# Performance work log

Hardware: AMD Instinct MI355X
Metric: run time of the kernel (lower is better)

Reference implementation:

```python
import jax, jax.numpy as jnp
import numpy as np

# Static problem sizes (uniform T/taus make the ragged edge list static).
B, N, F, T, TAU, S = 8, 384, 64, 192, 192, 5
SINK_SHIFT = T                    # min sink index == T (sinks are the new nodes)
N_SINK, N_SOURCE = TAU, T + TAU - 1


def _edge_indices():
    # tril_indices(T+tau, offset=-1), keep sink >= T  (window=None)
    r, c = np.tril_indices(T + TAU, k=-1)
    m = r >= T
    r, c = r[m], c[m]
    e = r.shape[0]
    batch = np.repeat(np.arange(B), e)
    return (jnp.asarray(batch, jnp.int32),
            jnp.asarray(np.tile(r, B), jnp.int32),
            jnp.asarray(np.tile(c, B), jnp.int32))


def setup_inputs() -> dict:
    key = jax.random.key(0)
    ks = jax.random.split(key, 6)
    batch_idx, sink_idx, source_idx = _edge_indices()
    s1, s2 = 1.0 / np.sqrt(2 * F), 1.0 / np.sqrt(F)
    return {
        "nodes": jax.random.normal(ks[0], (B, N, F), jnp.float32),
        "w1": jax.random.uniform(ks[1], (2 * F, F), jnp.float32, -s1, s1),
        "b1": jnp.zeros((F,), jnp.float32),
        "g1": jnp.ones((F,), jnp.float32),
        "be1": jnp.zeros((F,), jnp.float32),
        "w2": jax.random.uniform(ks[2], (F, F), jnp.float32, -s2, s2),
        "b2": jnp.zeros((F,), jnp.float32),
        "g2": jnp.ones((F,), jnp.float32),
        "be2": jnp.zeros((F,), jnp.float32),
        "w3": jax.random.uniform(ks[3], (F, 1), jnp.float32, -s2, s2),
        "b3": jnp.zeros((1,), jnp.float32),
        "gumbel": jax.random.gumbel(ks[4], (S, B, N_SINK, N_SOURCE), jnp.float32),
        "batch_idx": batch_idx,
        "sink_idx": sink_idx,
        "source_idx": source_idx,
    }


def _ln(x, g, b):
    mu = x.mean(-1, keepdims=True)
    v = ((x - mu) ** 2).mean(-1, keepdims=True)
    return (x - mu) * jax.lax.rsqrt(v + 1e-5) * g + b


def reference(nodes, w1, b1, g1, be1, w2, b2, g2, be2, w3, b3,
              gumbel, batch_idx, sink_idx, source_idx):
    # gather sink/source node pairs: [E, 2F]
    sink = nodes[batch_idx, sink_idx]
    src = nodes[batch_idx, source_idx]
    x = jnp.concatenate([sink, src], axis=-1)
    # edge MLP -> per-edge logit
    h = _ln(jax.nn.relu(x @ w1 + b1), g1, be1)
    h = _ln(jax.nn.relu(h @ w2 + b2), g2, be2)
    logits = (h @ w3 + b3)[:, 0]                     # [E]
    # dense-padded grid filled with finfo.min (as in torch)
    neg = jnp.finfo(jnp.float32).min
    gs = jnp.full((B, N_SINK, N_SOURCE), neg, jnp.float32)
    gs = gs.at[batch_idx, sink_idx - SINK_SHIFT, source_idx].set(logits)
    # hard gumbel-softmax over source dim, S independent samples
    y_soft = jax.nn.softmax(gs[None] + gumbel, axis=-1)      # [S,B,192,383]
    y_hard = jax.nn.one_hot(jnp.argmax(y_soft, -1), N_SOURCE, dtype=y_soft.dtype)
    y = y_soft + jax.lax.stop_gradient(y_hard - y_soft)
    e = y.sum(0)
    # straight-through binarize: forward (e>0), backward identity
    e = e + jax.lax.stop_gradient((e > 0).astype(e.dtype) - e)
    valid = e[batch_idx, sink_idx - SINK_SHIFT, source_idx]
    vals = jnp.where(valid > 0, valid, 0.0)
    # dense equivalent of the sparse COO adjacency (B, N, N)
    return jnp.zeros((B, N, N), jnp.float32).at[batch_idx, sink_idx, source_idx].set(vals)
```

## Files before the change

### kernel.cpp

```cpp
#include <hip/hip_runtime.h>
#include <math.h>
#include <stdint.h>

#define BB 8
#define NN 384
#define FF 64
#define TT 192
#define NSRC 383
#define NSINK 192
#define SS 5
#define NEDGE 441600
#define BN (BB * NN)
#define TILE_E 128
#define NBLKE (NEDGE / TILE_E)
#define OUTV ((BB * NN * NN) / 4)

typedef float f32x2 __attribute__((ext_vector_type(2)));

#if defined(__has_builtin) && __has_builtin(__builtin_elementwise_fma)
#define PKFMA(a, b, c) __builtin_elementwise_fma((a), (b), (c))
#else
#define PKFMA(a, b, c) ((a) * (b) + (c))
#endif

__global__ __launch_bounds__(64) void prep_all(
    const float* __restrict__ nodes, const float* __restrict__ w1,
    const float* __restrict__ b1,
    const float* __restrict__ w2, const float* __restrict__ b2,
    const float* __restrict__ g1, const float* __restrict__ be1,
    const float* __restrict__ g2, const float* __restrict__ be2,
    const float* __restrict__ w3, const float* __restrict__ b3,
    float* __restrict__ A, float* __restrict__ Bv,
    float* __restrict__ W2kj, float* __restrict__ wcol,
    float* __restrict__ cb, float* __restrict__ gw,
    float* __restrict__ cwsgw) {
  const int blk = blockIdx.x;
  const int k = threadIdx.x;
  if (blk < BN / 4) {
    const int bn0 = blk * 4;
    __shared__ float nd[4][FF];
#pragma unroll
    for (int i = 0; i < 4; ++i) nd[i][k] = nodes[(bn0 + i) * FF + k];
    __syncthreads();
    const float bk = b1[k];
    float a0 = bk, a1 = bk, a2 = bk, a3 = bk;
    float q0 = 0.f, q1 = 0.f, q2 = 0.f, q3 = 0.f;
#pragma unroll 8
    for (int f = 0; f < FF; ++f) {
      const float wt = w1[f * FF + k];
      const float wb = w1[(FF + f) * FF + k];
      const float n0 = nd[0][f], n1 = nd[1][f], n2 = nd[2][f], n3 = nd[3][f];
      a0 = fmaf(n0, wt, a0); a1 = fmaf(n1, wt, a1);
      a2 = fmaf(n2, wt, a2); a3 = fmaf(n3, wt, a3);
      q0 = fmaf(n0, wb, q0); q1 = fmaf(n1, wb, q1);
      q2 = fmaf(n2, wb, q2); q3 = fmaf(n3, wb, q3);
    }
    A[(bn0 + 0) * FF + k] = a0;  Bv[(bn0 + 0) * FF + k] = q0;
    A[(bn0 + 1) * FF + k] = a1;  Bv[(bn0 + 1) * FF + k] = q1;
    A[(bn0 + 2) * FF + k] = a2;  Bv[(bn0 + 2) * FF + k] = q2;
    A[(bn0 + 3) * FF + k] = a3;  Bv[(bn0 + 3) * FF + k] = q3;
  } else {
    const int j = k;
    float cbj = b2[j];
    float wc = 0.f;
    for (int kk = 0; kk < FF; ++kk) {
      const float wraw = w2[kk * FF + j];
      const float w = g1[kk] * wraw;
      W2kj[kk * FF + j] = w;
      wc += w;
      cbj = fmaf(be1[kk], wraw, cbj);
    }
    wcol[j] = wc;
    cb[j] = cbj;
    const float gwj = g2[j] * w3[j];
    gw[j] = gwj;
    __shared__ float sA[FF], sB[FF];
    sA[j] = gwj;
    sB[j] = be2[j] * w3[j];
    __syncthreads();
    if (j == 0) {
      float a = 0.f, bq = 0.f;
      for (int i = 0; i < FF; ++i) { a += sA[i]; bq += sB[i]; }
      cwsgw[0] = b3[0] + bq;
      cwsgw[1] = a;
    }
  }
}

__global__ __launch_bounds__(256, 4) void edge_mlp(
    const float* __restrict__ A, const float* __restrict__ Bv,
    const float* __restrict__ W2kj, const float* __restrict__ wcolg,
    const float* __restrict__ cbg, const float* __restrict__ gwg,
    const float* __restrict__ cwsgw,
    const int* __restrict__ bidx, const int* __restrict__ ridx,
    const int* __restrict__ cidx, float* __restrict__ L,
    float4* __restrict__ outv) {
  __shared__ float Wl[FF][FF];
  __shared__ float X[4][FF][32];
  __shared__ float St[4][32][2];

  const int tid = threadIdx.x;
  const int wave = tid >> 6;
  const int lane = tid & 63;
  const int gtid = blockIdx.x * 256 + tid;
  if (gtid < OUTV) outv[gtid] = make_float4(0.f, 0.f, 0.f, 0.f);

  const int e0 = blockIdx.x * TILE_E + wave * 32;

  {
    const float4* src = (const float4*)W2kj;
    float4* dst = (float4*)&Wl[0][0];
#pragma unroll
    for (int i = 0; i < 4; ++i) dst[tid + 256 * i] = src[tid + 256 * i];
  }

  const int joct = lane & 7;
  const int egs = lane >> 3;
  float wc[8], cbv[8], gwv[8];
  *(float4*)&wc[0] = *(const float4*)(wcolg + 8 * joct);
  *(float4*)&wc[4] = *(const float4*)(wcolg + 8 * joct + 4);
  *(float4*)&cbv[0] = *(const float4*)(cbg + 8 * joct);
  *(float4*)&cbv[4] = *(const float4*)(cbg + 8 * joct + 4);
  *(float4*)&gwv[0] = *(const float4*)(gwg + 8 * joct);
  *(float4*)&gwv[4] = *(const float4*)(gwg + 8 * joct + 4);
  const float cw = cwsgw[0], sgw = cwsgw[1];

  __syncthreads();

  {
    const int e = lane >> 1;
    const int kh = lane & 1;
    const int ge = e0 + e;
    const int b = bidx[ge], r = ridx[ge], c = cidx[ge];
    const float4* pa = (const float4*)(A + (b * NN + r) * FF + kh * 32);
    const float4* pb = (const float4*)(Bv + (b * NN + c) * FF + kh * 32);
    float s = 0.f, q = 0.f;
#pragma unroll
    for (int i = 0; i < 8; ++i) {
      const float4 av = pa[i];
      const float4 bv = pb[i];
      const float x0 = fmaxf(av.x + bv.x, 0.f);
      const float x1 = fmaxf(av.y + bv.y, 0.f);
      const float x2 = fmaxf(av.z + bv.z, 0.f);
      const float x3 = fmaxf(av.w + bv.w, 0.f);
      const int kb = kh * 32 + 4 * i;
      X[wave][kb + 0][e] = x0; X[wave][kb + 1][e] = x1;
      X[wave][kb + 2][e] = x2; X[wave][kb + 3][e] = x3;
      s += x0; s += x1; s += x2; s += x3;
      q = fmaf(x0, x0, q); q = fmaf(x1, x1, q);
      q = fmaf(x2, x2, q); q = fmaf(x3, x3, q);
    }
    s += __shfl_xor(s, 1, 64);
    q += __shfl_xor(q, 1, 64);
    const float mu = s * (1.f / FF);
    const float rstd = 1.f / sqrtf(q * (1.f / FF) - mu * mu + 1e-5f);
    St[wave][e][kh] = kh ? rstd : mu;
  }
  __builtin_amdgcn_wave_barrier();

  f32x2 t2[4][4];
#pragma unroll
  for (int ei = 0; ei < 4; ++ei)
#pragma unroll
    for (int p = 0; p < 4; ++p) t2[ei][p] = (f32x2){0.f, 0.f};

  const float* xp = &X[wave][0][4 * egs];
  const float* wp = &Wl[0][8 * joct];
#pragma unroll 8
  for (int k = 0; k < FF; ++k) {
    const float4 x4 = *(const float4*)xp;  xp += 32;
    const float4 wA = *(const float4*)wp;
    const float4 wB = *(const float4*)(wp + 4);  wp += 64;
    f32x2 w01; w01.x = wA.x; w01.y = wA.y;
    f32x2 w23; w23.x = wA.z; w23.y = wA.w;
    f32x2 w45; w45.x = wB.x; w45.y = wB.y;
    f32x2 w67; w67.x = wB.z; w67.y = wB.w;
    const float xe[4] = {x4.x, x4.y, x4.z, x4.w};
#pragma unroll
    for (int ei = 0; ei < 4; ++ei) {
      const float xs = xe[ei];
      f32x2 xb; xb.x = xs; xb.y = xs;
      t2[ei][0] = PKFMA(xb, w01, t2[ei][0]);
      t2[ei][1] = PKFMA(xb, w23, t2[ei][1]);
      t2[ei][2] = PKFMA(xb, w45, t2[ei][2]);
      t2[ei][3] = PKFMA(xb, w67, t2[ei][3]);
    }
  }

  float mu_[4], rs_[4];
#pragma unroll
  for (int ei = 0; ei < 4; ++ei) {
    mu_[ei] = St[wave][4 * egs + ei][0];
    rs_[ei] = St[wave][4 * egs + ei][1];
  }
  float s1[4], s2[4], s3[4];
#pragma unroll
  for (int ei = 0; ei < 4; ++ei) { s1[ei] = 0.f; s2[ei] = 0.f; s3[ei] = 0.f; }
#pragma unroll
  for (int ei = 0; ei < 4; ++ei) {
#pragma unroll
    for (int jj = 0; jj < 8; ++jj) {
      const float tv = (jj & 1) ? t2[ei][jj >> 1].y : t2[ei][jj >> 1].x;
      const float pre = fmaf(rs_[ei], fmaf(-mu_[ei], wc[jj], tv), cbv[jj]);
      const float tr = fmaxf(pre, 0.f);
      s1[ei] += tr;
      s2[ei] = fmaf(tr, tr, s2[ei]);
      s3[ei] = fmaf(tr, gwv[jj], s3[ei]);
    }
  }
#pragma unroll
  for (int off = 1; off <= 4; off <<= 1) {
#pragma unroll
    for (int ei = 0; ei < 4; ++ei) {
      s1[ei] += __shfl_xor(s1[ei], off, 64);
      s2[ei] += __shfl_xor(s2[ei], off, 64);
      s3[ei] += __shfl_xor(s3[ei], off, 64);
    }
  }
  if (joct < 4) {
    const int ei = joct;
    const int ge = e0 + 4 * egs + ei;
    const int b = bidx[ge], r = ridx[ge], c = cidx[ge];
    const float mu2 = s1[ei] * (1.f / FF);
    const float var2 = s2[ei] * (1.f / FF) - mu2 * mu2;
    const float rstd2 = 1.f / sqrtf(var2 + 1e-5f);
    const float logit = fmaf(rstd2, fmaf(-mu2, sgw, s3[ei]), cw);
    L[(b * NSINK + (r - TT)) * NSRC + c] = logit;
  }
}

__global__ __launch_bounds__(256) void argmax_scatter(
    const float* __restrict__ L, const float* __restrict__ gum,
    float* __restrict__ out) {
  const int task = blockIdx.x * 4 + (threadIdx.x >> 6);
  const int lane = threadIdx.x & 63;
  const int row = task % NSINK;
  const int sb = task / NSINK;
  const int b = sb & 7;
  const int r = row + TT;

  const float* __restrict__ lrow = L + (b * NSINK + row) * NSRC;
  const float* __restrict__ grow = gum + task * NSRC;

  float bv = -INFINITY;
  int bi = 0;
  for (int c = lane; c < r; c += 64) {
    const float v = lrow[c] + grow[c];
    if (v > bv) { bv = v; bi = c; }
  }
#pragma unroll
  for (int off = 32; off > 0; off >>= 1) {
    const float ov = __shfl_xor(bv, off, 64);
    const int oi = __shfl_xor(bi, off, 64);
    if (ov > bv || (ov == bv && oi < bi)) { bv = ov; bi = oi; }
  }
  if (lane == 0) out[(b * NN + r) * NN + bi] = 1.0f;
}

extern "C" void kernel_launch(void* const* d_in, const int* in_sizes, int n_in,
                              void* d_out, int out_size, void* d_ws, size_t ws_size,
                              hipStream_t stream) {
  const float* nodes = (const float*)d_in[0];
  const float* w1 = (const float*)d_in[1];
  const float* b1 = (const float*)d_in[2];
  const float* g1 = (const float*)d_in[3];
  const float* be1 = (const float*)d_in[4];
  const float* w2 = (const float*)d_in[5];
  const float* b2 = (const float*)d_in[6];
  const float* g2 = (const float*)d_in[7];
  const float* be2 = (const float*)d_in[8];
  const float* w3 = (const float*)d_in[9];
  const float* b3 = (const float*)d_in[10];
  const float* gum = (const float*)d_in[11];
  const int* bidx = (const int*)d_in[12];
  const int* ridx = (const int*)d_in[13];
  const int* cidx = (const int*)d_in[14];
  float* out = (float*)d_out;

  float* ws = (float*)d_ws;
  float* A = ws;
  float* Bv = A + BN * FF;
  float* W2kj = Bv + BN * FF;
  float* wcol = W2kj + FF * FF;
  float* cb = wcol + FF;
  float* gw = cb + FF;
  float* cwsgw = gw + FF;
  float* L = ws + 397520;
  (void)ws_size; (void)n_in; (void)in_sizes; (void)out_size;

  hipLaunchKernelGGL(prep_all, dim3(BN / 4 + 1), dim3(64), 0, stream,
                     nodes, w1, b1, w2, b2, g1, be1, g2, be2, w3, b3,
                     A, Bv, W2kj, wcol, cb, gw, cwsgw);
  hipLaunchKernelGGL(edge_mlp, dim3(NBLKE), dim3(256), 0, stream,
                     A, Bv, W2kj, wcol, cb, gw, cwsgw, bidx, ridx, cidx, L,
                     (float4*)out);
  hipLaunchKernelGGL(argmax_scatter, dim3((SS * BB * NSINK) / 4), dim3(256), 0, stream,
                     L, gum, out);
}
```

Before: 155.8 us.

## Double edge tile per wave and enlarge per-thread register tile in edge MLP

Each block of the edge MLP now handles 256 edges instead of 128, so each wave covers 64 edges. One thread gathers one whole edge row, and LayerNorm statistics stay in registers and are passed by shuffle rather than through shared memory. The second matmul now computes an 8-edge by 8-output register tile per thread, doubling reuse of each LDS weight and activation load. In exchange it needs more registers and about 80KB of LDS per block, with the occupancy hint lowered from 4 to 2 blocks. Each lane then picks its own edge's reduced sums with a select tree, so every lane writes one logit.

```diff
diff --git a/kernel.cpp b/kernel.cpp
--- a/kernel.cpp
+++ b/kernel.cpp
@@ -11,7 +11,7 @@
 #define SS 5
 #define NEDGE 441600
 #define BN (BB * NN)
-#define TILE_E 128
+#define TILE_E 256
 #define NBLKE (NEDGE / TILE_E)
 #define OUTV ((BB * NN * NN) / 4)
 
@@ -22,6 +22,11 @@
 #else
 #define PKFMA(a, b, c) ((a) * (b) + (c))
 #endif
+
+__device__ __forceinline__ float sel8(const float* s, int i) {
+  return (i & 4) ? ((i & 2) ? ((i & 1) ? s[7] : s[6]) : ((i & 1) ? s[5] : s[4]))
+                 : ((i & 2) ? ((i & 1) ? s[3] : s[2]) : ((i & 1) ? s[1] : s[0]));
+}
 
 __global__ __launch_bounds__(64) void prep_all(
     const float* __restrict__ nodes, const float* __restrict__ w1,
@@ -87,7 +92,7 @@
   }
 }
 
-__global__ __launch_bounds__(256, 4) void edge_mlp(
+__global__ __launch_bounds__(256, 2) void edge_mlp(
     const float* __restrict__ A, const float* __restrict__ Bv,
     const float* __restrict__ W2kj, const float* __restrict__ wcolg,
     const float* __restrict__ cbg, const float* __restrict__ gwg,
@@ -96,16 +101,14 @@
     const int* __restrict__ cidx, float* __restrict__ L,
     float4* __restrict__ outv) {
   __shared__ float Wl[FF][FF];
-  __shared__ float X[4][FF][32];
-  __shared__ float St[4][32][2];
+  __shared__ float X[4][FF][64];
 
   const int tid = threadIdx.x;
   const int wave = tid >> 6;
   const int lane = tid & 63;
+
   const int gtid = blockIdx.x * 256 + tid;
   if (gtid < OUTV) outv[gtid] = make_float4(0.f, 0.f, 0.f, 0.f);
-
-  const int e0 = blockIdx.x * TILE_E + wave * 32;
 
   {
     const float4* src = (const float4*)W2kj;
@@ -114,8 +117,69 @@
     for (int i = 0; i < 4; ++i) dst[tid + 256 * i] = src[tid + 256 * i];
   }
 
+  const int ge = blockIdx.x * TILE_E + tid;
+  const int b = bidx[ge], r = ridx[ge], c = cidx[ge];
+  float mu, rstd;
+  {
+    const float4* pa = (const float4*)(A + (b * NN + r) * FF);
+    const float4* pb = (const float4*)(Bv + (b * NN + c) * FF);
+    float s = 0.f, q = 0.f;
+#pragma unroll
+    for (int i = 0; i < 16; ++i) {
+      const float4 av = pa[i];
+      const float4 bv = pb[i];
+      const float x0 = fmaxf(av.x + bv.x, 0.f);
+      const float x1 = fmaxf(av.y + bv.y, 0.f);
+      const float x2 = fmaxf(av.z + bv.z, 0.f);
+      const float x3 = fmaxf(av.w + bv.w, 0.f);
+      const int kb = 4 * i;
+      X[wave][kb + 0][lane] = x0;
+      X[wave][kb + 1][lane] = x1;
+      X[wave][kb + 2][lane] = x2;
+      X[wave][kb + 3][lane] = x3;
+      s += x0; s += x1; s += x2; s += x3;
+      q = fmaf(x0, x0, q); q = fmaf(x1, x1, q);
+      q = fmaf(x2, x2, q); q = fmaf(x3, x3, q);
+    }
+    mu = s * (1.f / FF);
+    rstd = 1.f / sqrtf(q * (1.f / FF) - mu * mu + 1e-5f);
+  }
+
+  __syncthreads();
+
   const int joct = lane & 7;
-  const int egs = lane >> 3;
+  const int eg3 = lane >> 3;
+  f32x2 t2[8][4];
+#pragma unroll
+  for (int ei = 0; ei < 8; ++ei)
+#pragma unroll
+    for (int p = 0; p < 4; ++p) t2[ei][p] = (f32x2){0.f, 0.f};
+
+  const float* xrow = &X[wave][0][8 * eg3];
+  const float* wrow = &Wl[0][8 * joct];
+#pragma unroll 4
+  for (int k = 0; k < FF; ++k) {
+    const float4 xA = *(const float4*)xrow;
+    const float4 xB = *(const float4*)(xrow + 4);
+    xrow += 64;
+    const float4 wA = *(const float4*)wrow;
+    const float4 wB = *(const float4*)(wrow + 4);
+    wrow += 64;
+    f32x2 w01; w01.x = wA.x; w01.y = wA.y;
+    f32x2 w23; w23.x = wA.z; w23.y = wA.w;
+    f32x2 w45; w45.x = wB.x; w45.y = wB.y;
+    f32x2 w67; w67.x = wB.z; w67.y = wB.w;
+    const float xe[8] = {xA.x, xA.y, xA.z, xA.w, xB.x, xB.y, xB.z, xB.w};
+#pragma unroll
+    for (int ei = 0; ei < 8; ++ei) {
+      f32x2 xb; xb.x = xe[ei]; xb.y = xe[ei];
+      t2[ei][0] = PKFMA(xb, w01, t2[ei][0]);
+      t2[ei][1] = PKFMA(xb, w23, t2[ei][1]);
+      t2[ei][2] = PKFMA(xb, w45, t2[ei][2]);
+      t2[ei][3] = PKFMA(xb, w67, t2[ei][3]);
+    }
+  }
+
   float wc[8], cbv[8], gwv[8];
   *(float4*)&wc[0] = *(const float4*)(wcolg + 8 * joct);
   *(float4*)&wc[4] = *(const float4*)(wcolg + 8 * joct + 4);
@@ -125,108 +189,41 @@
   *(float4*)&gwv[4] = *(const float4*)(gwg + 8 * joct + 4);
   const float cw = cwsgw[0], sgw = cwsgw[1];
 
-  __syncthreads();
-
-  {
-    const int e = lane >> 1;
-    const int kh = lane & 1;
-    const int ge = e0 + e;
-    const int b = bidx[ge], r = ridx[ge], c = cidx[ge];
-    const float4* pa = (const float4*)(A + (b * NN + r) * FF + kh * 32);
-    const float4* pb = (const float4*)(Bv + (b * NN + c) * FF + kh * 32);
-    float s = 0.f, q = 0.f;
-#pragma unroll
-    for (int i = 0; i < 8; ++i) {
-      const float4 av = pa[i];
-      const float4 bv = pb[i];
-      const float x0 = fmaxf(av.x + bv.x, 0.f);
-      const float x1 = fmaxf(av.y + bv.y, 0.f);
-      const float x2 = fmaxf(av.z + bv.z, 0.f);
-      const float x3 = fmaxf(av.w + bv.w, 0.f);
-      const int kb = kh * 32 + 4 * i;
-      X[wave][kb + 0][e] = x0; X[wave][kb + 1][e] = x1;
-      X[wave][kb + 2][e] = x2; X[wave][kb + 3][e] = x3;
-      s += x0; s += x1; s += x2; s += x3;
-      q = fmaf(x0, x0, q); q = fmaf(x1, x1, q);
-      q = fmaf(x2, x2, q); q = fmaf(x3, x3, q);
-    }
-    s += __shfl_xor(s, 1, 64);
-    q += __shfl_xor(q, 1, 64);
-    const float mu = s * (1.f / FF);
-    const float rstd = 1.f / sqrtf(q * (1.f / FF) - mu * mu + 1e-5f);
-    St[wave][e][kh] = kh ? rstd : mu;
-  }
-  __builtin_amdgcn_wave_barrier();
-
-  f32x2 t2[4][4];
-#pragma unroll
-  for (int ei = 0; ei < 4; ++ei)
-#pragma unroll
-    for (int p = 0; p < 4; ++p) t2[ei][p] = (f32x2){0.f, 0.f};
-
-  const float* xp = &X[wave][0][4 * egs];
-  const float* wp = &Wl[0][8 * joct];
-#pragma unroll 8
-  for (int k = 0; k < FF; ++k) {
-    const float4 x4 = *(const float4*)xp;  xp += 32;
-    const float4 wA = *(const float4*)wp;
-    const float4 wB = *(const float4*)(wp + 4);  wp += 64;
-    f32x2 w01; w01.x = wA.x; w01.y = wA.y;
-    f32x2 w23; w23.x = wA.z; w23.y = wA.w;
-    f32x2 w45; w45.x = wB.x; w45.y = wB.y;
-    f32x2 w67; w67.x = wB.z; w67.y = wB.w;
-    const float xe[4] = {x4.x, x4.y, x4.z, x4.w};
-#pragma unroll
-    for (int ei = 0; ei < 4; ++ei) {
-      const float xs = xe[ei];
-      f32x2 xb; xb.x = xs; xb.y = xs;
-      t2[ei][0] = PKFMA(xb, w01, t2[ei][0]);
-      t2[ei][1] = PKFMA(xb, w23, t2[ei][1]);
-      t2[ei][2] = PKFMA(xb, w45, t2[ei][2]);
-      t2[ei][3] = PKFMA(xb, w67, t2[ei][3]);
-    }
-  }
-
-  float mu_[4], rs_[4];
-#pragma unroll
-  for (int ei = 0; ei < 4; ++ei) {
-    mu_[ei] = St[wave][4 * egs + ei][0];
-    rs_[ei] = St[wave][4 * egs + ei][1];
-  }
-  float s1[4], s2[4], s3[4];
-#pragma unroll
-  for (int ei = 0; ei < 4; ++ei) { s1[ei] = 0.f; s2[ei] = 0.f; s3[ei] = 0.f; }
-#pragma unroll
-  for (int ei = 0; ei < 4; ++ei) {
+  const int base8 = lane & 56;
+  float s1[8], s2[8], s3[8];
+#pragma unroll
+  for (int ei = 0; ei < 8; ++ei) {
+    const float m = __shfl(mu, base8 + ei, 64);
+    const float rs = __shfl(rstd, base8 + ei, 64);
+    float a1 = 0.f, a2 = 0.f, a3 = 0.f;
 #pragma unroll
     for (int jj = 0; jj < 8; ++jj) {
       const float tv = (jj & 1) ? t2[ei][jj >> 1].y : t2[ei][jj >> 1].x;
-      const float pre = fmaf(rs_[ei], fmaf(-mu_[ei], wc[jj], tv), cbv[jj]);
+      const float pre = fmaf(rs, fmaf(-m, wc[jj], tv), cbv[jj]);
       const float tr = fmaxf(pre, 0.f);
-      s1[ei] += tr;
-      s2[ei] = fmaf(tr, tr, s2[ei]);
-      s3[ei] = fmaf(tr, gwv[jj], s3[ei]);
-    }
+      a1 += tr;
+      a2 = fmaf(tr, tr, a2);
+      a3 = fmaf(tr, gwv[jj], a3);
+    }
+    s1[ei] = a1; s2[ei] = a2; s3[ei] = a3;
   }
 #pragma unroll
   for (int off = 1; off <= 4; off <<= 1) {
 #pragma unroll
-    for (int ei = 0; ei < 4; ++ei) {
+    for (int ei = 0; ei < 8; ++ei) {
       s1[ei] += __shfl_xor(s1[ei], off, 64);
       s2[ei] += __shfl_xor(s2[ei], off, 64);
       s3[ei] += __shfl_xor(s3[ei], off, 64);
     }
   }
-  if (joct < 4) {
-    const int ei = joct;
-    const int ge = e0 + 4 * egs + ei;
-    const int b = bidx[ge], r = ridx[ge], c = cidx[ge];
-    const float mu2 = s1[ei] * (1.f / FF);
-    const float var2 = s2[ei] * (1.f / FF) - mu2 * mu2;
-    const float rstd2 = 1.f / sqrtf(var2 + 1e-5f);
-    const float logit = fmaf(rstd2, fmaf(-mu2, sgw, s3[ei]), cw);
-    L[(b * NSINK + (r - TT)) * NSRC + c] = logit;
-  }
+  const float S1 = sel8(s1, joct);
+  const float S2 = sel8(s2, joct);
+  const float S3 = sel8(s3, joct);
+  const float mu2 = S1 * (1.f / FF);
+  const float var2 = S2 * (1.f / FF) - mu2 * mu2;
+  const float rstd2 = 1.f / sqrtf(var2 + 1e-5f);
+  const float logit = fmaf(rstd2, fmaf(-mu2, sgw, S3), cw);
+  L[(b * NSINK + (r - TT)) * NSRC + c] = logit;
 }
 
 __global__ __launch_bounds__(256) void argmax_scatter(
```

Measured after the change: 153.6 us. About the same (-1.4%).
